# Kernel tuning notes

Hardware: AMD Instinct MI355X
Metric: run time of the kernel (lower is better)

The kernel has to match this reference:

```python
import jax, jax.numpy as jnp
import numpy as np

B = 64
N_CTRL_PLANES = 512
CPD = 64          # control_plane_dim
NF = 256          # n_frames
WS = 512          # window_size (SSM per-frame output size)
SD = 128          # state_dim
NS = NF * WS // 2 # 65536 output samples (overlap-add hop = WS//2)
TOP_K = 8


def setup_inputs() -> dict:
    key = jax.random.key(0)
    ks = jax.random.split(key, 8)
    return {
        "control_plane_choice": jax.random.normal(ks[0], (B, N_CTRL_PLANES), dtype=jnp.float32),
        "times": jax.random.normal(ks[1], (B, 1, NF), dtype=jnp.float32),
        # Lookup.items, initialized uniform(-1, 1)
        "lookup_items": jax.random.uniform(ks[2], (N_CTRL_PLANES, CPD * NF), dtype=jnp.float32, minval=-1.0, maxval=1.0),
        # SSM parameters, initialized uniform(-0.01, 0.01)
        "proj": jax.random.uniform(ks[3], (CPD, WS), dtype=jnp.float32, minval=-0.01, maxval=0.01),
        "state_matrix": jax.random.uniform(ks[4], (SD, SD), dtype=jnp.float32, minval=-0.01, maxval=0.01),
        "input_matrix": jax.random.uniform(ks[5], (WS, SD), dtype=jnp.float32, minval=-0.01, maxval=0.01),
        "output_matrix": jax.random.uniform(ks[6], (SD, WS), dtype=jnp.float32, minval=-0.01, maxval=0.01),
        "direct_matrix": jax.random.uniform(ks[7], (WS, WS), dtype=jnp.float32, minval=-0.01, maxval=0.01),
    }


def _sparse_softmax_onehot(x, axis=-1):
    # softmax then hard one-hot at the argmax with value 1 (normalize=True variant)
    sm = jax.nn.softmax(x, axis=axis)
    return (sm == jnp.max(sm, axis=axis, keepdims=True)).astype(x.dtype)


def _fft_convolve(a, b):
    # linear convolution via zero-padding to 2N, truncated back to N
    n = a.shape[-1]
    fa = jnp.fft.rfft(jnp.pad(a, ((0, 0), (0, 0), (0, n))), axis=-1)
    fb = jnp.fft.rfft(jnp.pad(b, ((0, 0), (0, 0), (0, n))), axis=-1)
    return jnp.fft.irfft(fa * fb, axis=-1)[..., :n]


def reference(control_plane_choice, times, lookup_items, proj, state_matrix, input_matrix, output_matrix, direct_matrix):
    batch = control_plane_choice.shape[0]
    cpd, ws = proj.shape
    nf = lookup_items.shape[1] // cpd
    sd = state_matrix.shape[0]
    hop = ws // 2
    ns = nf * hop

    # --- Lookup with sparse_softmax selection (hard one-hot @ items) ---
    sel = _sparse_softmax_onehot(control_plane_choice, axis=-1)   # (B, n_items)
    cp = sel @ lookup_items                                       # (B, cpd*nf)

    # --- softmax over flattened control plane, then top-8 sparsify ---
    cp = jax.nn.softmax(cp, axis=-1)                              # (B, cpd*nf)
    vals, idx = jax.lax.top_k(cp, TOP_K)                          # (B, 8)
    cp = jnp.zeros_like(cp).at[jnp.arange(batch)[:, None], idx].set(vals)
    cp = cp.reshape(batch, cpd, nf)

    # --- windowed SSM: linear state-space recurrence over frames ---
    inp = jnp.einsum('bcf,cw->fbw', cp, proj)                     # (nf, B, ws)

    def step(state, x):  # state: (B, sd), x: (B, ws)
        state = state @ state_matrix + x @ input_matrix
        out = state @ output_matrix + x @ direct_matrix
        return state, out

    state0 = jnp.zeros((batch, sd), dtype=cp.dtype)
    _, outs = jax.lax.scan(step, state0, inp)                     # (nf, B, ws)
    frames = jnp.transpose(outs, (1, 0, 2))                       # (B, nf, ws)

    # --- overlap-add with Hann window, hop = ws//2 ---
    n_ = jnp.arange(ws, dtype=cp.dtype)
    window = 0.5 * (1.0 - jnp.cos(2.0 * jnp.pi * n_ / ws))        # periodic Hann
    win_frames = frames * window
    oa_idx = jnp.arange(nf)[:, None] * hop + jnp.arange(ws)[None, :]
    sig = jnp.zeros((batch, nf * hop + ws), dtype=cp.dtype).at[:, oa_idx].add(win_frames)
    samples = sig[:, :ns][:, None, :]                             # (B, 1, ns)

    # --- Dirac scheduler: one-hot times -> upsample with holes -> fft convolve ---
    t_oh = _sparse_softmax_onehot(times, axis=-1)                 # (B, 1, nf)
    factor = ns // nf
    impulses = jnp.zeros((batch, 1, ns), dtype=cp.dtype).at[:, :, ::factor].set(t_oh)
    return _fft_convolve(samples, impulses)                       # (B, 1, ns)
```

## Files before the change

### kernel.cpp

```cpp
#include <hip/hip_runtime.h>
#include <math.h>

#define NBATCH 64
#define NCP    512
#define CPD    64
#define NF     256
#define WSZ    512
#define SD     128
#define NSAMP  65536
#define TPROP  8
#define NSLICE 8
#define SLICE_ELEMS 2048

__device__ __forceinline__ bool better(float v1, int i1, float v2, int i2) {
  return (v1 > v2) || (v1 == v2 && i1 < i2);
}

__device__ __forceinline__ void cswap(float& v1, int& i1, float& v2, int& i2) {
  if (better(v2, i2, v1, i1)) {
    float tv = v1; v1 = v2; v2 = tv;
    int   ti = i1; i1 = i2; i2 = ti;
  }
}

__device__ __forceinline__ void wave_argmax(float& v, int& i) {
#pragma unroll
  for (int off = 32; off > 0; off >>= 1) {
    float ov = __shfl_down(v, off);
    int   oi = __shfl_down(i, off);
    if (better(ov, oi, v, i)) { v = ov; i = oi; }
  }
}

__device__ __forceinline__ void xor_merge8(float* m, int* mi, int off) {
  float lb[8]; int ib8[8];
#pragma unroll
  for (int k = 0; k < 8; k++) { lb[k] = __shfl_xor(m[k], off); ib8[k] = __shfl_xor(mi[k], off); }
  float x[8]; int xi[8];
#pragma unroll
  for (int k = 0; k < 8; k++) {
    const bool ta = better(m[k], mi[k], lb[7 - k], ib8[7 - k]);
    x[k]  = ta ? m[k]  : lb[7 - k];
    xi[k] = ta ? mi[k] : ib8[7 - k];
  }
  cswap(x[0], xi[0], x[4], xi[4]); cswap(x[1], xi[1], x[5], xi[5]);
  cswap(x[2], xi[2], x[6], xi[6]); cswap(x[3], xi[3], x[7], xi[7]);
  cswap(x[0], xi[0], x[2], xi[2]); cswap(x[1], xi[1], x[3], xi[3]);
  cswap(x[4], xi[4], x[6], xi[6]); cswap(x[5], xi[5], x[7], xi[7]);
  cswap(x[0], xi[0], x[1], xi[1]); cswap(x[2], xi[2], x[3], xi[3]);
  cswap(x[4], xi[4], x[5], xi[5]); cswap(x[6], xi[6], x[7], xi[7]);
#pragma unroll
  for (int k = 0; k < 8; k++) { m[k] = x[k]; mi[k] = xi[k]; }
}

__global__ __launch_bounds__(256) void k_scan(
    const float* __restrict__ cpc, const float* __restrict__ times,
    const float* __restrict__ lookup,
    const float* __restrict__ proj, const float* __restrict__ Amat,
    const float* __restrict__ Bmat,
    float* __restrict__ S,
    float* __restrict__ pmax, float* __restrict__ psum,
    float* __restrict__ pcv, int* __restrict__ pci,
    int* __restrict__ pshift) {
  const int t = threadIdx.x;
  const int bid = blockIdx.x;

  __shared__ float wred[4];
  __shared__ int   wredi[4];
  __shared__ int   sRow;
  __shared__ float wlv[32];
  __shared__ int   wli[32];
  __shared__ float sSmax;
  __shared__ float pr[WSZ];
  __shared__ float sred[256];
  __shared__ float sb[2][SD];

  if (bid >= NBATCH * NSLICE) {
    const int c = bid - NBATCH * NSLICE;
    if (t < 128) ((float4*)pr)[t] = ((const float4*)(proj + (size_t)c * WSZ))[t];
    __syncthreads();
    const int d = t & 127, h = t >> 7;
    {
      float acc[8] = {0.f, 0.f, 0.f, 0.f, 0.f, 0.f, 0.f, 0.f};
      const float* Bp  = Bmat + (size_t)(h * 256) * SD + d;
      const float* prh = pr + h * 256;
#pragma unroll 4
      for (int kb = 0; kb < 256; kb += 8) {
        const float4 p0 = *(const float4*)(prh + kb);
        const float4 p1 = *(const float4*)(prh + kb + 4);
        acc[0] = fmaf(p0.x, Bp[(size_t)(kb + 0) * SD], acc[0]);
        acc[1] = fmaf(p0.y, Bp[(size_t)(kb + 1) * SD], acc[1]);
        acc[2] = fmaf(p0.z, Bp[(size_t)(kb + 2) * SD], acc[2]);
        acc[3] = fmaf(p0.w, Bp[(size_t)(kb + 3) * SD], acc[3]);
        acc[4] = fmaf(p1.x, Bp[(size_t)(kb + 4) * SD], acc[4]);
        acc[5] = fmaf(p1.y, Bp[(size_t)(kb + 5) * SD], acc[5]);
        acc[6] = fmaf(p1.z, Bp[(size_t)(kb + 6) * SD], acc[6]);
        acc[7] = fmaf(p1.w, Bp[(size_t)(kb + 7) * SD], acc[7]);
      }
      sred[t] = ((acc[0] + acc[1]) + (acc[2] + acc[3])) + ((acc[4] + acc[5]) + (acc[6] + acc[7]));
    }
    __syncthreads();
    if (t < SD) sb[0][t] = sred[t] + sred[t + 128];
    __syncthreads();
    int cur = 0;
    for (int j = 0; j < TPROP; j++) {
      if (t < SD) S[((size_t)j * CPD + c) * SD + t] = sb[cur][t];
      float acc[8] = {0.f, 0.f, 0.f, 0.f, 0.f, 0.f, 0.f, 0.f};
      const float* Ap = Amat + (size_t)(h * 64) * SD + d;
      const float* sh = sb[cur] + h * 64;
#pragma unroll
      for (int ib = 0; ib < 64; ib += 8) {
        const float4 s0v = *(const float4*)(sh + ib);
        const float4 s1v = *(const float4*)(sh + ib + 4);
        acc[0] = fmaf(s0v.x, Ap[(size_t)(ib + 0) * SD], acc[0]);
        acc[1] = fmaf(s0v.y, Ap[(size_t)(ib + 1) * SD], acc[1]);
        acc[2] = fmaf(s0v.z, Ap[(size_t)(ib + 2) * SD], acc[2]);
        acc[3] = fmaf(s0v.w, Ap[(size_t)(ib + 3) * SD], acc[3]);
        acc[4] = fmaf(s1v.x, Ap[(size_t)(ib + 4) * SD], acc[4]);
        acc[5] = fmaf(s1v.y, Ap[(size_t)(ib + 5) * SD], acc[5]);
        acc[6] = fmaf(s1v.z, Ap[(size_t)(ib + 6) * SD], acc[6]);
        acc[7] = fmaf(s1v.w, Ap[(size_t)(ib + 7) * SD], acc[7]);
      }
      sred[t] = ((acc[0] + acc[1]) + (acc[2] + acc[3])) + ((acc[4] + acc[5]) + (acc[6] + acc[7]));
      __syncthreads();
      if (t < SD) sb[cur ^ 1][t] = sred[t] + sred[t + 128];
      __syncthreads();
      cur ^= 1;
    }
    return;
  }

  const int b = bid >> 3, s = bid & 7;
  const int lane = t & 63, wv = t >> 6;

  {
    float v0 = cpc[b * NCP + t];
    float v1 = cpc[b * NCP + t + 256];
    float bv = v0; int bi = t;
    if (better(v1, t + 256, bv, bi)) { bv = v1; bi = t + 256; }
    wave_argmax(bv, bi);
    if (lane == 0) { wred[wv] = bv; wredi[wv] = bi; }
    __syncthreads();
    if (t == 0) {
      float fv = wred[0]; int fi = wredi[0];
#pragma unroll
      for (int q = 1; q < 4; q++)
        if (better(wred[q], wredi[q], fv, fi)) { fv = wred[q]; fi = wredi[q]; }
      sRow = fi;
    }
    __syncthreads();
  }
  const float* row = lookup + (size_t)sRow * (CPD * NF);
  const float4* row4 = (const float4*)(row + s * SLICE_ELEMS);

  const float4 va = row4[t];
  const float4 vb = row4[t + 256];
  const int gbase = s * SLICE_ELEMS;
  float ev[8] = {va.x, va.y, va.z, va.w, vb.x, vb.y, vb.z, vb.w};
  int   ei[8] = {gbase + t * 4,        gbase + t * 4 + 1,
                 gbase + t * 4 + 2,    gbase + t * 4 + 3,
                 gbase + 1024 + t * 4, gbase + 1024 + t * 4 + 1,
                 gbase + 1024 + t * 4 + 2, gbase + 1024 + t * 4 + 3};

  float m[8]; int mi[8];
#pragma unroll
  for (int k = 0; k < 8; k++) { m[k] = ev[k]; mi[k] = ei[k]; }
#pragma unroll
  for (int i = 0; i < 7; i++)
#pragma unroll
    for (int j = 0; j < 7 - i; j++) cswap(m[j], mi[j], m[j + 1], mi[j + 1]);

  xor_merge8(m, mi, 1);  xor_merge8(m, mi, 2);  xor_merge8(m, mi, 4);
  xor_merge8(m, mi, 8);  xor_merge8(m, mi, 16); xor_merge8(m, mi, 32);

  if (lane < 8) { wlv[wv * 8 + lane] = m[lane]; wli[wv * 8 + lane] = mi[lane]; }
  __syncthreads();

  if (wv == 0) {
    float v = (lane < 32) ? wlv[lane] : -3.4e38f;
    int   i = (lane < 32) ? wli[lane] : 0x7fffffff;
#pragma unroll
    for (int k = 2; k <= 32; k <<= 1) {
#pragma unroll
      for (int j = k >> 1; j > 0; j >>= 1) {
        const float pv = __shfl_xor(v, j);
        const int   pi = __shfl_xor(i, j);
        const bool keepBetter = (((lane & k) == 0) == ((lane & j) == 0));
        if (keepBetter == better(pv, pi, v, i)) { v = pv; i = pi; }
      }
    }
    if (lane == 0) sSmax = v;
    if (lane < 8) { pcv[b * 64 + s * 8 + lane] = v; pci[b * 64 + s * 8 + lane] = i; }
  }
  __syncthreads();
  const float smax = sSmax;

  float se = 0.f;
#pragma unroll
  for (int k = 0; k < 8; k++) se += __expf(ev[k] - smax);
#pragma unroll
  for (int off = 32; off > 0; off >>= 1) se += __shfl_down(se, off);
  if (lane == 0) wred[wv] = se;
  __syncthreads();
  if (t == 0) {
    pmax[b * 8 + s] = smax;
    psum[b * 8 + s] = (wred[0] + wred[1]) + (wred[2] + wred[3]);
  }

  if (s == 0) {
    float tv = times[b * NF + t]; int ti = t;
    wave_argmax(tv, ti);
    if (lane == 0) { wred[wv] = tv; wredi[wv] = ti; }
    __syncthreads();
    if (t == 0) {
      float fv = wred[0]; int fi = wredi[0];
#pragma unroll
      for (int q = 1; q < 4; q++)
        if (better(wred[q], wredi[q], fv, fi)) { fv = wred[q]; fi = wredi[q]; }
      pshift[b] = fi * (NSAMP / NF);
    }
  }
}

__global__ __launch_bounds__(256) void k_expand(
    const float* __restrict__ proj, const float* __restrict__ Cmat,
    const float* __restrict__ Dmat, const float* __restrict__ S,
    const float* __restrict__ pmax, const float* __restrict__ psum,
    const float* __restrict__ pcv, const int* __restrict__ pci,
    float* __restrict__ P2, float* __restrict__ R,
    float* __restrict__ vals, int* __restrict__ cidx, int* __restrict__ fidx) {
  const int t = threadIdx.x;
  const int bid = blockIdx.x;
  __shared__ float sh[WSZ];

  if (bid < TPROP * CPD * 2) {
    const int jc = bid >> 1;
    const int wbase = (bid & 1) * 256;
    if (t < SD) sh[t] = S[(size_t)jc * SD + t];
    __syncthreads();
    float acc = 0.f;
    const float* Cp = Cmat + wbase + t;
#pragma unroll 8
    for (int i = 0; i < SD; i++) acc += sh[i] * Cp[i * WSZ];
    R[(size_t)jc * WSZ + wbase + t] = acc;
  } else if (bid < TPROP * CPD * 2 + CPD * 2) {
    const int pid = bid - TPROP * CPD * 2;
    const int c = pid >> 1;
    const int wbase = (pid & 1) * 256;
    for (int i = t; i < WSZ; i += 256) sh[i] = proj[c * WSZ + i];
    __syncthreads();
    float acc = 0.f;
    const float* Dp = Dmat + wbase + t;
#pragma unroll 8
    for (int u = 0; u < WSZ; u++) acc += sh[u] * Dp[u * WSZ];
    P2[(size_t)c * WSZ + wbase + t] = acc;
  } else {
    const int b = bid - (TPROP * CPD * 2 + CPD * 2);
    if (t < 64) {
      const int sl = t >> 3;
      float M = pmax[b * 8 + sl];
#pragma unroll
      for (int off = 1; off < 64; off <<= 1) M = fmaxf(M, __shfl_xor(M, off));
      float ps = ((t & 7) == 0) ? psum[b * 8 + sl] * __expf(pmax[b * 8 + sl] - M) : 0.f;
#pragma unroll
      for (int off = 1; off < 64; off <<= 1) ps += __shfl_xor(ps, off);
      float cvv = pcv[b * 64 + t]; int cii = pci[b * 64 + t];
      for (int p = 0; p < 8; p++) {
        float v = cvv; int i = cii;
#pragma unroll
        for (int off = 1; off < 64; off <<= 1) {
          float ov = __shfl_xor(v, off); int oi = __shfl_xor(i, off);
          if (better(ov, oi, v, i)) { v = ov; i = oi; }
        }
        if (t == 0) {
          vals[b * 8 + p] = __expf(v - M) / ps;
          cidx[b * 8 + p] = i / NF;
          fidx[b * 8 + p] = i % NF;
        }
        if (cii == i) cvv = -3.4e38f;
      }
    }
  }
}

__global__ __launch_bounds__(256) void k_out(
    const float* __restrict__ vals, const int* __restrict__ cidx,
    const int* __restrict__ fidx, const int* __restrict__ pshift,
    const float* __restrict__ P2, const float* __restrict__ R,
    float* __restrict__ out) {
  const int b = blockIdx.x >> 6;
  const int chunk = blockIdx.x & 63;
  const int t = threadIdx.x;
  const int n = chunk * 1024 + t * 4;
  const int m = n - pshift[b];
  float o[4] = {0.f, 0.f, 0.f, 0.f};
  if (m >= 0) {
    const int f1 = m >> 8;
    const int w1 = m & 255;
    float a[4] = {0.f, 0.f, 0.f, 0.f};
    float g[4] = {0.f, 0.f, 0.f, 0.f};
    const bool hasf2 = (f1 > 0);
#pragma unroll
    for (int k = 0; k < 8; k++) {
      const float v = vals[b * 8 + k];
      const int c = cidx[b * 8 + k];
      const int d1 = f1 - fidx[b * 8 + k];
      if (d1 >= 0 && d1 < TPROP) {
        const float4 q = *(const float4*)(R + ((size_t)(d1 * CPD + c)) * WSZ + w1);
        a[0] += v * q.x; a[1] += v * q.y; a[2] += v * q.z; a[3] += v * q.w;
      }
      if (d1 == 0) {
        const float4 q = *(const float4*)(P2 + (size_t)c * WSZ + w1);
        a[0] += v * q.x; a[1] += v * q.y; a[2] += v * q.z; a[3] += v * q.w;
      }
      if (hasf2) {
        const int d2 = d1 - 1;
        if (d2 >= 0 && d2 < TPROP) {
          const float4 q = *(const float4*)(R + ((size_t)(d2 * CPD + c)) * WSZ + w1 + 256);
          g[0] += v * q.x; g[1] += v * q.y; g[2] += v * q.z; g[3] += v * q.w;
        }
        if (d2 == 0) {
          const float4 q = *(const float4*)(P2 + (size_t)c * WSZ + w1 + 256);
          g[0] += v * q.x; g[1] += v * q.y; g[2] += v * q.z; g[3] += v * q.w;
        }
      }
    }
    const float k2pi = 6.283185307179586f / (float)WSZ;
#pragma unroll
    for (int i = 0; i < 4; i++) {
      const float cs = __cosf(k2pi * (float)(w1 + i));
      const float wa = 0.5f * (1.f - cs);
      const float wb = 0.5f * (1.f + cs);
      o[i] = wa * a[i] + wb * g[i];
    }
  }
  float4 ov = make_float4(o[0], o[1], o[2], o[3]);
  *(float4*)(out + (size_t)b * NSAMP + n) = ov;
}

extern "C" void kernel_launch(void* const* d_in, const int* in_sizes, int n_in,
                              void* d_out, int out_size, void* d_ws, size_t ws_size,
                              hipStream_t stream) {
  const float* cpc    = (const float*)d_in[0];
  const float* times  = (const float*)d_in[1];
  const float* lookup = (const float*)d_in[2];
  const float* proj   = (const float*)d_in[3];
  const float* Amat   = (const float*)d_in[4];
  const float* Bmat   = (const float*)d_in[5];
  const float* Cmat   = (const float*)d_in[6];
  const float* Dmat   = (const float*)d_in[7];
  float* out = (float*)d_out;

  float* w      = (float*)d_ws;
  float* vals   = w;
  int*   cidx   = (int*)(w + 512);
  int*   fidx   = (int*)(w + 1024);
  int*   pshift = (int*)(w + 1536);
  float* P2     = w + 1600;
  float* R      = P2 + CPD * WSZ;
  float* S      = R + (size_t)TPROP * CPD * WSZ;
  float* pmax   = S + (size_t)TPROP * CPD * SD;
  float* psum   = pmax + NBATCH * NSLICE;
  float* pcv    = psum + NBATCH * NSLICE;
  int*   pci    = (int*)(pcv + NBATCH * NSLICE * 8);

  hipLaunchKernelGGL(k_scan, dim3(NBATCH * NSLICE + CPD), dim3(256), 0, stream,
                     cpc, times, lookup, proj, Amat, Bmat,
                     S, pmax, psum, pcv, pci, pshift);
  hipLaunchKernelGGL(k_expand, dim3(TPROP * CPD * 2 + CPD * 2 + NBATCH), dim3(256), 0, stream,
                     proj, Cmat, Dmat, S, pmax, psum, pcv, pci,
                     P2, R, vals, cidx, fidx);
  hipLaunchKernelGGL(k_out, dim3(NBATCH * 64), dim3(256), 0, stream,
                     vals, cidx, fidx, pshift, P2, R, out);
}
```

Before: 141.5 us.

## Stage state matrix in LDS, reorder scan blocks, and batch expand matmuls over four rows

The SSM state-propagation blocks now load the 128x128 state matrix into shared memory once and iterate from LDS instead of global memory. They are also moved to the front of the grid so the long serial chains start first. In the expand kernel, each block now computes four rows of the proj@D and S@C products, reusing every loaded matrix element four times and cutting block count. The price is 64KB of LDS for every k_scan block, including the selection blocks, which may reduce occupancy there.

Measured after the change: 139.9 us. Within noise of the previous version (-1.1%).

```diff
diff --git a/kernel.cpp b/kernel.cpp
--- a/kernel.cpp
+++ b/kernel.cpp
@@ -65,63 +65,58 @@
   const int t = threadIdx.x;
   const int bid = blockIdx.x;
 
+  __shared__ __align__(16) float Alds[SD * SD];
+  __shared__ float sb[2][SD];
+  __shared__ float sred[256];
   __shared__ float wred[4];
   __shared__ int   wredi[4];
   __shared__ int   sRow;
   __shared__ float wlv[32];
   __shared__ int   wli[32];
   __shared__ float sSmax;
-  __shared__ float pr[WSZ];
-  __shared__ float sred[256];
-  __shared__ float sb[2][SD];
-
-  if (bid >= NBATCH * NSLICE) {
-    const int c = bid - NBATCH * NSLICE;
-    if (t < 128) ((float4*)pr)[t] = ((const float4*)(proj + (size_t)c * WSZ))[t];
-    __syncthreads();
+
+  if (bid < CPD) {
+    const int c = bid;
+    for (int i = t; i < SD * SD / 4; i += 256)
+      ((float4*)Alds)[i] = ((const float4*)Amat)[i];
+
     const int d = t & 127, h = t >> 7;
     {
-      float acc[8] = {0.f, 0.f, 0.f, 0.f, 0.f, 0.f, 0.f, 0.f};
-      const float* Bp  = Bmat + (size_t)(h * 256) * SD + d;
-      const float* prh = pr + h * 256;
-#pragma unroll 4
-      for (int kb = 0; kb < 256; kb += 8) {
-        const float4 p0 = *(const float4*)(prh + kb);
-        const float4 p1 = *(const float4*)(prh + kb + 4);
-        acc[0] = fmaf(p0.x, Bp[(size_t)(kb + 0) * SD], acc[0]);
-        acc[1] = fmaf(p0.y, Bp[(size_t)(kb + 1) * SD], acc[1]);
-        acc[2] = fmaf(p0.z, Bp[(size_t)(kb + 2) * SD], acc[2]);
-        acc[3] = fmaf(p0.w, Bp[(size_t)(kb + 3) * SD], acc[3]);
-        acc[4] = fmaf(p1.x, Bp[(size_t)(kb + 4) * SD], acc[4]);
-        acc[5] = fmaf(p1.y, Bp[(size_t)(kb + 5) * SD], acc[5]);
-        acc[6] = fmaf(p1.z, Bp[(size_t)(kb + 6) * SD], acc[6]);
-        acc[7] = fmaf(p1.w, Bp[(size_t)(kb + 7) * SD], acc[7]);
-      }
-      sred[t] = ((acc[0] + acc[1]) + (acc[2] + acc[3])) + ((acc[4] + acc[5]) + (acc[6] + acc[7]));
+      const float* Bp = Bmat + (size_t)(h * 256) * SD + d;
+      const float* pv = proj + (size_t)c * WSZ + h * 256;
+      float acc[16];
+#pragma unroll
+      for (int k = 0; k < 16; k++) acc[k] = 0.f;
+#pragma unroll 2
+      for (int kb = 0; kb < 256; kb += 16) {
+#pragma unroll
+        for (int u = 0; u < 16; u++)
+          acc[u] = fmaf(pv[kb + u], Bp[(size_t)(kb + u) * SD], acc[u]);
+      }
+      float s8 = 0.f;
+#pragma unroll
+      for (int k = 0; k < 16; k++) s8 += acc[k];
+      sred[t] = s8;
     }
     __syncthreads();
     if (t < SD) sb[0][t] = sred[t] + sred[t + 128];
     __syncthreads();
+
     int cur = 0;
     for (int j = 0; j < TPROP; j++) {
       if (t < SD) S[((size_t)j * CPD + c) * SD + t] = sb[cur][t];
-      float acc[8] = {0.f, 0.f, 0.f, 0.f, 0.f, 0.f, 0.f, 0.f};
-      const float* Ap = Amat + (size_t)(h * 64) * SD + d;
+      float a0 = 0.f, a1 = 0.f, a2 = 0.f, a3 = 0.f;
+      const float* Ah = Alds + (size_t)(h * 64) * SD + d;
       const float* sh = sb[cur] + h * 64;
 #pragma unroll
-      for (int ib = 0; ib < 64; ib += 8) {
-        const float4 s0v = *(const float4*)(sh + ib);
-        const float4 s1v = *(const float4*)(sh + ib + 4);
-        acc[0] = fmaf(s0v.x, Ap[(size_t)(ib + 0) * SD], acc[0]);
-        acc[1] = fmaf(s0v.y, Ap[(size_t)(ib + 1) * SD], acc[1]);
-        acc[2] = fmaf(s0v.z, Ap[(size_t)(ib + 2) * SD], acc[2]);
-        acc[3] = fmaf(s0v.w, Ap[(size_t)(ib + 3) * SD], acc[3]);
-        acc[4] = fmaf(s1v.x, Ap[(size_t)(ib + 4) * SD], acc[4]);
-        acc[5] = fmaf(s1v.y, Ap[(size_t)(ib + 5) * SD], acc[5]);
-        acc[6] = fmaf(s1v.z, Ap[(size_t)(ib + 6) * SD], acc[6]);
-        acc[7] = fmaf(s1v.w, Ap[(size_t)(ib + 7) * SD], acc[7]);
-      }
-      sred[t] = ((acc[0] + acc[1]) + (acc[2] + acc[3])) + ((acc[4] + acc[5]) + (acc[6] + acc[7]));
+      for (int i = 0; i < 64; i += 4) {
+        const float4 sv = *(const float4*)(sh + i);
+        a0 = fmaf(sv.x, Ah[(size_t)(i + 0) * SD], a0);
+        a1 = fmaf(sv.y, Ah[(size_t)(i + 1) * SD], a1);
+        a2 = fmaf(sv.z, Ah[(size_t)(i + 2) * SD], a2);
+        a3 = fmaf(sv.w, Ah[(size_t)(i + 3) * SD], a3);
+      }
+      sred[t] = (a0 + a1) + (a2 + a3);
       __syncthreads();
       if (t < SD) sb[cur ^ 1][t] = sred[t] + sred[t + 128];
       __syncthreads();
@@ -130,7 +125,8 @@
     return;
   }
 
-  const int b = bid >> 3, s = bid & 7;
+  const int sbid = bid - CPD;
+  const int b = sbid >> 3, s = sbid & 7;
   const int lane = t & 63, wv = t >> 6;
 
   {
@@ -231,31 +227,49 @@
     float* __restrict__ vals, int* __restrict__ cidx, int* __restrict__ fidx) {
   const int t = threadIdx.x;
   const int bid = blockIdx.x;
-  __shared__ float sh[WSZ];
-
-  if (bid < TPROP * CPD * 2) {
-    const int jc = bid >> 1;
+  __shared__ __align__(16) float xsh[4 * WSZ];
+
+  if (bid < CPD / 4 * 2) {
+    const int g = bid >> 1;
     const int wbase = (bid & 1) * 256;
-    if (t < SD) sh[t] = S[(size_t)jc * SD + t];
-    __syncthreads();
-    float acc = 0.f;
+    for (int i = t; i < 4 * WSZ; i += 256) xsh[i] = proj[(size_t)(4 * g) * WSZ + i];
+    __syncthreads();
+    float a0 = 0.f, a1 = 0.f, a2 = 0.f, a3 = 0.f;
+    const float* Dp = Dmat + wbase + t;
+#pragma unroll 8
+    for (int u = 0; u < WSZ; u++) {
+      const float dv = Dp[(size_t)u * WSZ];
+      a0 = fmaf(xsh[u], dv, a0);
+      a1 = fmaf(xsh[WSZ + u], dv, a1);
+      a2 = fmaf(xsh[2 * WSZ + u], dv, a2);
+      a3 = fmaf(xsh[3 * WSZ + u], dv, a3);
+    }
+    P2[(size_t)(4 * g + 0) * WSZ + wbase + t] = a0;
+    P2[(size_t)(4 * g + 1) * WSZ + wbase + t] = a1;
+    P2[(size_t)(4 * g + 2) * WSZ + wbase + t] = a2;
+    P2[(size_t)(4 * g + 3) * WSZ + wbase + t] = a3;
+  } else if (bid < 32 + TPROP * CPD / 4 * 2) {
+    const int rb = bid - 32;
+    const int g = rb >> 1;
+    const int wbase = (rb & 1) * 256;
+    for (int i = t; i < 4 * SD; i += 256) xsh[i] = S[(size_t)(4 * g) * SD + i];
+    __syncthreads();
+    float a0 = 0.f, a1 = 0.f, a2 = 0.f, a3 = 0.f;
     const float* Cp = Cmat + wbase + t;
 #pragma unroll 8
-    for (int i = 0; i < SD; i++) acc += sh[i] * Cp[i * WSZ];
-    R[(size_t)jc * WSZ + wbase + t] = acc;
-  } else if (bid < TPROP * CPD * 2 + CPD * 2) {
-    const int pid = bid - TPROP * CPD * 2;
-    const int c = pid >> 1;
-    const int wbase = (pid & 1) * 256;
-    for (int i = t; i < WSZ; i += 256) sh[i] = proj[c * WSZ + i];
-    __syncthreads();
-    float acc = 0.f;
-    const float* Dp = Dmat + wbase + t;
-#pragma unroll 8
-    for (int u = 0; u < WSZ; u++) acc += sh[u] * Dp[u * WSZ];
-    P2[(size_t)c * WSZ + wbase + t] = acc;
+    for (int i = 0; i < SD; i++) {
+      const float cv = Cp[(size_t)i * WSZ];
+      a0 = fmaf(xsh[i], cv, a0);
+      a1 = fmaf(xsh[SD + i], cv, a1);
+      a2 = fmaf(xsh[2 * SD + i], cv, a2);
+      a3 = fmaf(xsh[3 * SD + i], cv, a3);
+    }
+    R[(size_t)(4 * g + 0) * WSZ + wbase + t] = a0;
+    R[(size_t)(4 * g + 1) * WSZ + wbase + t] = a1;
+    R[(size_t)(4 * g + 2) * WSZ + wbase + t] = a2;
+    R[(size_t)(4 * g + 3) * WSZ + wbase + t] = a3;
   } else {
-    const int b = bid - (TPROP * CPD * 2 + CPD * 2);
+    const int b = bid - (32 + TPROP * CPD / 4 * 2);
     if (t < 64) {
       const int sl = t >> 3;
       float M = pmax[b * 8 + sl];
@@ -364,10 +378,10 @@
   float* pcv    = psum + NBATCH * NSLICE;
   int*   pci    = (int*)(pcv + NBATCH * NSLICE * 8);
 
-  hipLaunchKernelGGL(k_scan, dim3(NBATCH * NSLICE + CPD), dim3(256), 0, stream,
+  hipLaunchKernelGGL(k_scan, dim3(CPD + NBATCH * NSLICE), dim3(256), 0, stream,
                      cpc, times, lookup, proj, Amat, Bmat,
                      S, pmax, psum, pcv, pci, pshift);
-  hipLaunchKernelGGL(k_expand, dim3(TPROP * CPD * 2 + CPD * 2 + NBATCH), dim3(256), 0, stream,
+  hipLaunchKernelGGL(k_expand, dim3(32 + TPROP * CPD / 4 * 2 + NBATCH), dim3(256), 0, stream,
                      proj, Cmat, Dmat, S, pmax, psum, pcv, pci,
                      P2, R, vals, cidx, fidx);
   hipLaunchKernelGGL(k_out, dim3(NBATCH * 64), dim3(256), 0, stream,
```
